# Kernel optimization log

Measured on AMD Instinct MI355X. Metric: run time of the kernel, lower is better.

The kernel has to match this reference:

```python
import jax, jax.numpy as jnp
import numpy as np
from jax import lax


def _conv(x, w, b, pad):
    # x: [B,C,H,W], w: [O,I,kh,kw]
    y = lax.conv_general_dilated(x, w, (1, 1), [(pad, pad), (pad, pad)],
                                 dimension_numbers=('NCHW', 'OIHW', 'NCHW'))
    return y + b[None, :, None, None]


def _maxpool2(x):
    return lax.reduce_window(x, -jnp.inf, lax.max, (1, 1, 2, 2), (1, 1, 2, 2), 'VALID')


def setup_inputs() -> dict:
    key = jax.random.key(0)
    ks = jax.random.split(key, 6)
    N, T, R, D = 8, 64, 9, 512
    x = jax.random.normal(ks[0], (N, T, R, D), dtype=jnp.float32)
    x = x / jnp.linalg.norm(x, axis=-1, keepdims=True)  # ViSiL features are L2-normalized
    w1 = jax.random.normal(ks[1], (32, 1, 3, 3), dtype=jnp.float32) * 0.05
    w2 = jax.random.normal(ks[2], (64, 32, 3, 3), dtype=jnp.float32) * 0.05
    w3 = jax.random.normal(ks[3], (128, 64, 3, 3), dtype=jnp.float32) * 0.05
    w4 = jax.random.normal(ks[4], (1, 128, 1, 1), dtype=jnp.float32) * 0.05
    return {
        'x': x,
        'w1': w1, 'b1': jnp.zeros((32,), jnp.float32),
        'w2': w2, 'b2': jnp.zeros((64,), jnp.float32),
        'w3': w3, 'b3': jnp.zeros((128,), jnp.float32),
        'w4': w4, 'b4': jnp.zeros((1,), jnp.float32),
    }


def reference(x, w1, b1, w2, b2, w3, b3, w4, b4):
    N, T, R, D = x.shape
    # frame-to-frame similarity: region correlation volume + chamfer (max over p, mean over o)
    sim = jnp.einsum('aiok,bjpk->aiopjb', x, x)        # [a,i,o,p,j,b]
    sim = jnp.mean(jnp.max(sim, axis=3), axis=2)        # [a,i,j,b]
    sim = jnp.transpose(sim, (0, 3, 1, 2)).reshape(N * N, 1, T, T)  # '(a b) () i j'
    # VideoComparator CNN head (ZeroPad2d(1) + valid 3x3 conv == 'same' 3x3 conv)
    h = jax.nn.relu(_conv(sim, w1, b1, 1))
    h = _maxpool2(h)
    h = jax.nn.relu(_conv(h, w2, b2, 1))
    h = _maxpool2(h)
    h = jax.nn.relu(_conv(h, w3, b3, 1))
    h = _conv(h, w4, b4, 0)                              # [N*N, 1, T/4, T/4]
    # SimilarityRegularizationLoss(min_val=-1, max_val=1)
    loss = jnp.sum(jax.nn.relu(-(h + 1.0))) + jnp.sum(jax.nn.relu(h - 1.0))
    # Hardtanh, rescale to [0,1], then video-to-video chamfer
    s = jnp.clip(h, -1.0, 1.0) / 2.0 + 0.5
    s = jnp.mean(jnp.max(s, axis=3), axis=2)             # [N*N, 1]
    return s.reshape(N, N), loss
```

## Files before the change

kernel.cpp:

```cpp
#include <hip/hip_runtime.h>

typedef unsigned short u16;
typedef unsigned int u32;
typedef __bf16 bf16x8 __attribute__((ext_vector_type(8)));
typedef u16 u16x8 __attribute__((ext_vector_type(8)));
typedef float f32x4 __attribute__((ext_vector_type(4)));

__device__ __forceinline__ u16 f2bf(float f) {
  u32 u = __float_as_uint(f);
  u32 r = (u + 0x7FFFu + ((u >> 16) & 1u)) >> 16;
  return (u16)r;
}

__device__ __forceinline__ void gload16(const void* g, void* l) {
  typedef __attribute__((address_space(1))) const void gvoid;
  typedef __attribute__((address_space(3))) void lvoid;
  __builtin_amdgcn_global_load_lds((gvoid*)g, (lvoid*)l, 16, 0, 0);
}

__global__ void k_cast(const float* __restrict__ x, char* __restrict__ A8,
                       const float* __restrict__ w2, const float* __restrict__ w3,
                       u16* __restrict__ p2, u16* __restrict__ p3,
                       float* __restrict__ out) {
  int t = blockIdx.x * 256 + threadIdx.x;
  const float4* xp = (const float4*)x + (size_t)t * 2;
  float4 v0 = xp[0], v1 = xp[1];
  int p0 = __builtin_amdgcn_cvt_pk_fp8_f32(v0.x, v0.y, 0, 0);
  p0 = __builtin_amdgcn_cvt_pk_fp8_f32(v0.z, v0.w, p0, 1);
  int p1 = __builtin_amdgcn_cvt_pk_fp8_f32(v1.x, v1.y, 0, 0);
  p1 = __builtin_amdgcn_cvt_pk_fp8_f32(v1.z, v1.w, p1, 1);
  ((int2*)A8)[t] = make_int2(p0, p1);
  if (blockIdx.x == 0 && threadIdx.x < 65) out[threadIdx.x] = 0.f;
  if (t < 18432) {
    int tt = t >> 11, oc = (t >> 5) & 63, ic = t & 31;
    p2[t] = f2bf(w2[(oc * 32 + ic) * 9 + tt]);
  }
  if (t < 73728) {
    int tt = t >> 13, oc = (t >> 6) & 127, ic = t & 63;
    p3[t] = f2bf(w3[(oc * 64 + ic) * 9 + tt]);
  }
}

__global__ __launch_bounds__(256) void k_gemm_smax(const char* __restrict__ A8,
                                                   float* __restrict__ Smax,
                                                   float* __restrict__ Sx) {
  __shared__ char smem[33792];
  float* slab = (float*)smem;
  const int chunk = blockIdx.x & 7, ci = blockIdx.x >> 3;
  const int csz = (chunk < 2) ? 84 : 83;
  if (ci >= csz) return;
  const int tlin = ((chunk < 2) ? 84 * chunk : 168 + 83 * (chunk - 2)) + ci;
  int rb = (int)((73.0f - sqrtf((float)(5329 - 8 * tlin))) * 0.5f);
  while (rb * 36 - rb * (rb - 1) / 2 > tlin) --rb;
  while ((rb + 1) * 36 - (rb + 1) * rb / 2 <= tlin) ++rb;
  const int cb = rb + (tlin - (rb * 36 - rb * (rb - 1) / 2));
  const int rowBase = rb * 128, colBase = cb * 128;
  const int tid = threadIdx.x, wave = tid >> 6, lane = tid & 63;
  const int lr = lane >> 2, lc = lane & 3;
  const int xs = (lr >> 1) & 3;
  const int lrow = lane & 15, lk = lane >> 4;
  const int xr = (lrow >> 1) & 3;
  const int wr = (wave & 1) * 64, wc = (wave >> 1) * 64;

  f32x4 acc[4][4];
#pragma unroll
  for (int rt = 0; rt < 4; ++rt)
#pragma unroll
    for (int ct = 0; ct < 4; ++ct) { f32x4 z = {0.f, 0.f, 0.f, 0.f}; acc[rt][ct] = z; }

  {
    char* As = smem;
    char* Bs = smem + 8192;
#pragma unroll
    for (int ii = 0; ii < 2; ++ii) {
      int r0 = wave * 32 + ii * 16;
      gload16(A8 + (size_t)(rowBase + r0 + lr) * 512 + ((lc ^ xs) * 16), As + r0 * 64);
      gload16(A8 + (size_t)(colBase + r0 + lr) * 512 + ((lc ^ xs) * 16), Bs + r0 * 64);
    }
  }
  __syncthreads();
  for (int k = 0; k < 8; ++k) {
    if (k < 7) {
      char* base = smem + (((k + 1) & 1) << 14);
      char* As = base;
      char* Bs = base + 8192;
      int k0 = (k + 1) * 64;
#pragma unroll
      for (int ii = 0; ii < 2; ++ii) {
        int r0 = wave * 32 + ii * 16;
        gload16(A8 + (size_t)(rowBase + r0 + lr) * 512 + k0 + ((lc ^ xs) * 16),
                As + r0 * 64);
        gload16(A8 + (size_t)(colBase + r0 + lr) * 512 + k0 + ((lc ^ xs) * 16),
                Bs + r0 * 64);
      }
    }
    {
      char* base = smem + ((k & 1) << 14);
      const char* As = base;
      const char* Bs = base + 8192;
#pragma unroll
      for (int s = 0; s < 2; ++s) {
        long af[4], bf[4];
#pragma unroll
        for (int rt = 0; rt < 4; ++rt) {
          int cc = s * 4 + lk;
          int sw = (((cc >> 1) ^ xr) * 16) + ((cc & 1) * 8);
          af[rt] = *(const long*)(As + (wr + rt * 16 + lrow) * 64 + sw);
        }
#pragma unroll
        for (int ct = 0; ct < 4; ++ct) {
          int cc = s * 4 + lk;
          int sw = (((cc >> 1) ^ xr) * 16) + ((cc & 1) * 8);
          bf[ct] = *(const long*)(Bs + (wc + ct * 16 + lrow) * 64 + sw);
        }
#pragma unroll
        for (int rt = 0; rt < 4; ++rt)
#pragma unroll
          for (int ct = 0; ct < 4; ++ct)
            acc[rt][ct] = __builtin_amdgcn_mfma_f32_16x16x32_fp8_fp8(
                af[rt], bf[ct], acc[rt][ct], 0, 0, 0);
      }
    }
    __syncthreads();
  }

  const int g0c = colBase / 9, offc = colBase % 9;
  const int g0r = rowBase / 9, offr = rowBase % 9;
  const int nph = (rb == cb) ? 2 : 4;
  for (int ph = 0; ph < nph; ++ph) {
    __syncthreads();
    if (ph < 2) {
      if ((wave & 1) == ph) {
#pragma unroll
        for (int rt = 0; rt < 4; ++rt)
#pragma unroll
          for (int ct = 0; ct < 4; ++ct)
#pragma unroll
            for (int r = 0; r < 4; ++r)
              slab[(rt * 16 + lk * 4 + r) * 129 + wc + ct * 16 + lrow] = acc[rt][ct][r];
      }
    } else {
      if ((wave >> 1) == ph - 2) {
#pragma unroll
        for (int rt = 0; rt < 4; ++rt)
#pragma unroll
          for (int ct = 0; ct < 4; ++ct)
#pragma unroll
            for (int r = 0; r < 4; ++r)
              slab[(ct * 16 + lrow) * 129 + wr + rt * 16 + lk * 4 + r] = acc[rt][ct][r];
      }
    }
    __syncthreads();
    for (int it = tid; it < 1024; it += 256) {
      int line = it >> 4, s = it & 15;
      float m = -3.0e38f;
      if (ph < 2) {
        int g = g0c + s;
        int cs = 9 * g - colBase, ce = cs + 9;
        cs = cs < 0 ? 0 : cs;
        ce = ce > 128 ? 128 : ce;
        if (cs >= ce) continue;
        const float* p = slab + line * 129;
        for (int c = cs; c < ce; ++c) m = fmaxf(m, p[c]);
        int r = rowBase + ph * 64 + line;
        if (s == 0 && offc != 0) Sx[(size_t)r * 36 + (cb - 1)] = m;
        else Smax[(size_t)r * 512 + g] = m;
      } else {
        int g = g0r + s;
        int rs = 9 * g - rowBase, re = rs + 9;
        rs = rs < 0 ? 0 : rs;
        re = re > 128 ? 128 : re;
        if (rs >= re) continue;
        const float* p = slab + line * 129;
        for (int r2 = rs; r2 < re; ++r2) m = fmaxf(m, p[r2]);
        int cgl = colBase + (ph - 2) * 64 + line;
        if (s == 0 && offr != 0) Sx[(size_t)cgl * 36 + (rb - 1)] = m;
        else Smax[(size_t)cgl * 512 + g] = m;
      }
    }
  }
}

__global__ void k_reduce_o(const float* __restrict__ Smax, const float* __restrict__ Sx,
                           float* __restrict__ sim) {
  int idx = blockIdx.x * 256 + threadIdx.x;
  int j = idx & 63, i = (idx >> 6) & 63, b = (idx >> 12) & 7, a = idx >> 15;
  int g = b * 64 + j;
  int t9 = 9 * g;
  int k = (t9 + 8) >> 7;
  bool part = ((u32)(128 * k - t9 - 1) < 8u);
  const float* p = Smax + (size_t)(a * 576 + i * 9) * 512 + g;
  const float* q = Sx + (size_t)(a * 576 + i * 9) * 36 + (k - 1);
  float s = 0.f;
#pragma unroll
  for (int o = 0; o < 9; ++o) {
    float v = p[o * 512];
    if (part) v = fmaxf(v, q[o * 36]);
    s += v;
  }
  sim[idx] = s * (1.f / 9.f);
}

__global__ __launch_bounds__(256) void k_conv1pool(const float* __restrict__ sim,
                                                   const float* __restrict__ w1,
                                                   const float* __restrict__ b1,
                                                   u16* __restrict__ h1) {
  __shared__ float tin[4096];
  const int pair = blockIdx.x, ocg = blockIdx.y, tid = threadIdx.x;
  const float4* src = (const float4*)(sim + (size_t)pair * 4096);
  for (int i = tid; i < 1024; i += 256) ((float4*)tin)[i] = src[i];
  __syncthreads();
  float wv[8][9], bs[8];
#pragma unroll
  for (int o = 0; o < 8; ++o) {
#pragma unroll
    for (int q = 0; q < 9; ++q) wv[o][q] = w1[(ocg * 8 + o) * 9 + q];
    bs[o] = b1[ocg * 8 + o];
  }
  for (int pp = tid; pp < 1024; pp += 256) {
    int py = pp >> 5, px = pp & 31;
    float m[8];
#pragma unroll
    for (int o = 0; o < 8; ++o) m[o] = 0.f;
#pragma unroll
    for (int dy = 0; dy < 2; ++dy)
#pragma unroll
      for (int dx = 0; dx < 2; ++dx) {
        float s[8];
#pragma unroll
        for (int o = 0; o < 8; ++o) s[o] = bs[o];
        int yy = py * 2 + dy, xx0 = px * 2 + dx;
#pragma unroll
        for (int ky = 0; ky < 3; ++ky) {
          int y = yy + ky - 1;
          if ((unsigned)y < 64u) {
#pragma unroll
            for (int kx = 0; kx < 3; ++kx) {
              int x = xx0 + kx - 1;
              if ((unsigned)x < 64u) {
                float v = tin[y * 64 + x];
#pragma unroll
                for (int o = 0; o < 8; ++o) s[o] += wv[o][ky * 3 + kx] * v;
              }
            }
          }
        }
#pragma unroll
        for (int o = 0; o < 8; ++o) m[o] = fmaxf(m[o], fmaxf(s[o], 0.f));
      }
    u16x8 r;
#pragma unroll
    for (int o = 0; o < 8; ++o) r[o] = f2bf(m[o]);
    *(u16x8*)&h1[(((size_t)pair * 32 + py) * 32 + px) * 32 + ocg * 8] = r;
  }
}

__global__ __launch_bounds__(256) void k_conv2pool(const u16* __restrict__ h1,
                                                   const u16* __restrict__ wp2,
                                                   const float* __restrict__ b2,
                                                   u16* __restrict__ h2) {
  __shared__ u16 tile[18 * 34 * 40];
  const int pair = blockIdx.x, yh = blockIdx.y, tid = threadIdx.x;
  const int wave = tid >> 6, lane = tid & 63, l15 = lane & 15, quad = lane >> 4;
  u16x8 z8 = {0, 0, 0, 0, 0, 0, 0, 0};
  for (int i = tid; i < 3060; i += 256) ((u16x8*)tile)[i] = z8;
  __syncthreads();
  for (int f = tid; f < 1152; f += 256) {
    int i = f >> 6, rem = f & 63, px = rem >> 1, half = rem & 1;
    int gr = yh * 16 - 1 + i;
    if ((unsigned)gr < 32u)
      *(u16x8*)&tile[(i * 34 + 1 + px) * 40 + half * 16] =
          *(const u16x8*)&h1[(((size_t)pair * 32 + gr) * 32 + px) * 32 + half * 16];
  }
  __syncthreads();

  f32x4 acc[8][4];
#pragma unroll
  for (int m = 0; m < 8; ++m)
#pragma unroll
    for (int n = 0; n < 4; ++n) { f32x4 z = {0.f, 0.f, 0.f, 0.f}; acc[m][n] = z; }

  for (int t = 0; t < 9; ++t) {
    int ky = t / 3, kx = t % 3;
    bf16x8 wf[4];
#pragma unroll
    for (int nt = 0; nt < 4; ++nt)
      wf[nt] = *(const bf16x8*)&wp2[((t * 64 + nt * 16 + l15) << 5) + quad * 8];
#pragma unroll
    for (int rr = 0; rr < 4; ++rr)
#pragma unroll
      for (int xh = 0; xh < 2; ++xh) {
        int lr = wave * 4 + rr;
        bf16x8 af = *(const bf16x8*)&tile[((lr + ky) * 34 + xh * 16 + l15 + kx) * 40 +
                                          quad * 8];
#pragma unroll
        for (int nt = 0; nt < 4; ++nt)
          acc[rr * 2 + xh][nt] =
              __builtin_amdgcn_mfma_f32_16x16x32_bf16(af, wf[nt], acc[rr * 2 + xh][nt],
                                                      0, 0, 0);
      }
  }

  float bv[4];
#pragma unroll
  for (int nt = 0; nt < 4; ++nt) bv[nt] = b2[nt * 16 + l15];
#pragma unroll
  for (int rp = 0; rp < 2; ++rp)
#pragma unroll
    for (int xh = 0; xh < 2; ++xh) {
      int py = yh * 8 + wave * 2 + rp;
      int px0 = xh * 8 + quad * 2;
#pragma unroll
      for (int nt = 0; nt < 4; ++nt) {
        f32x4 va = acc[(rp * 2) * 2 + xh][nt], vb = acc[(rp * 2 + 1) * 2 + xh][nt];
        float p0 = fmaxf(fmaxf(fmaxf(va[0], va[1]), fmaxf(vb[0], vb[1])) + bv[nt], 0.f);
        float p1 = fmaxf(fmaxf(fmaxf(va[2], va[3]), fmaxf(vb[2], vb[3])) + bv[nt], 0.f);
        size_t base = (((size_t)pair * 16 + py) * 16 + px0) * 64 + nt * 16 + l15;
        h2[base] = f2bf(p0);
        h2[base + 64] = f2bf(p1);
      }
    }
}

__global__ __launch_bounds__(256) void k_conv34(const u16* __restrict__ h2,
                                                const u16* __restrict__ wp3,
                                                const float* __restrict__ b3,
                                                const float* __restrict__ w4,
                                                const float* __restrict__ b4,
                                                float* __restrict__ out) {
  __shared__ u16 tile[18 * 18 * 72];
  __shared__ float lrow[16];
  __shared__ float lsw[4];
  const int pair = blockIdx.x, tid = threadIdx.x;
  const int wave = tid >> 6, lane = tid & 63, l15 = lane & 15, quad = lane >> 4;
  u16x8 z8 = {0, 0, 0, 0, 0, 0, 0, 0};
  for (int i = tid; i < 2916; i += 256) ((u16x8*)tile)[i] = z8;
  __syncthreads();
  for (int f = tid; f < 2048; f += 256) {
    int row = f >> 7, rem = f & 127, px = rem >> 3, seg = rem & 7;
    *(u16x8*)&tile[((row + 1) * 18 + px + 1) * 72 + seg * 8] =
        *(const u16x8*)&h2[(((size_t)pair * 16 + row) * 16 + px) * 64 + seg * 8];
  }
  __syncthreads();

  f32x4 acc[4][8];
#pragma unroll
  for (int m = 0; m < 4; ++m)
#pragma unroll
    for (int n = 0; n < 8; ++n) { f32x4 z = {0.f, 0.f, 0.f, 0.f}; acc[m][n] = z; }

  for (int t = 0; t < 9; ++t) {
    int ky = t / 3, kx = t % 3;
#pragma unroll
    for (int s = 0; s < 2; ++s) {
      bf16x8 wf[8];
#pragma unroll
      for (int nt = 0; nt < 8; ++nt)
        wf[nt] = *(const bf16x8*)&wp3[((t * 128 + nt * 16 + l15) << 6) + s * 32 +
                                      quad * 8];
#pragma unroll
      for (int yt = 0; yt < 4; ++yt) {
        int y = wave * 4 + yt;
        bf16x8 af = *(const bf16x8*)&tile[((y + ky) * 18 + l15 + kx) * 72 + s * 32 +
                                          quad * 8];
#pragma unroll
        for (int nt = 0; nt < 8; ++nt)
          acc[yt][nt] = __builtin_amdgcn_mfma_f32_16x16x32_bf16(af, wf[nt],
                                                                acc[yt][nt], 0, 0, 0);
      }
    }
  }

  float w4r[8], bvv[8];
#pragma unroll
  for (int nt = 0; nt < 8; ++nt) {
    w4r[nt] = w4[nt * 16 + l15];
    bvv[nt] = b3[nt * 16 + l15];
  }
  float b4v = b4[0];
  float lossacc = 0.f;
#pragma unroll
  for (int yt = 0; yt < 4; ++yt) {
    float hp[4] = {0.f, 0.f, 0.f, 0.f};
#pragma unroll
    for (int nt = 0; nt < 8; ++nt)
#pragma unroll
      for (int r = 0; r < 4; ++r)
        hp[r] += w4r[nt] * fmaxf(acc[yt][nt][r] + bvv[nt], 0.f);
#pragma unroll
    for (int off = 1; off <= 8; off <<= 1)
#pragma unroll
      for (int r = 0; r < 4; ++r) hp[r] += __shfl_xor(hp[r], off, 16);
    float rmax = 0.f, lw = 0.f;
#pragma unroll
    for (int r = 0; r < 4; ++r) {
      float h = hp[r] + b4v;
      lw += fmaxf(-(h + 1.f), 0.f) + fmaxf(h - 1.f, 0.f);
      float sc = fminf(fmaxf(h, -1.f), 1.f) * 0.5f + 0.5f;
      rmax = fmaxf(rmax, sc);
    }
    rmax = fmaxf(rmax, __shfl_xor(rmax, 16));
    rmax = fmaxf(rmax, __shfl_xor(rmax, 32));
    if (lane == 0) lrow[wave * 4 + yt] = rmax;
    lossacc += lw;
  }
#pragma unroll
  for (int off = 32; off >= 1; off >>= 1) lossacc += __shfl_xor(lossacc, off);
  if (lane == 0) lsw[wave] = lossacc * (1.f / 16.f);
  __syncthreads();
  if (tid == 0) {
    float mean = 0.f;
#pragma unroll
    for (int i = 0; i < 16; ++i) mean += lrow[i];
    out[pair] = mean * (1.f / 16.f);
    atomicAdd(out + 64, lsw[0] + lsw[1] + lsw[2] + lsw[3]);
  }
}

extern "C" void kernel_launch(void* const* d_in, const int* in_sizes, int n_in,
                              void* d_out, int out_size, void* d_ws, size_t ws_size,
                              hipStream_t stream) {
  (void)in_sizes; (void)n_in; (void)out_size; (void)ws_size;
  const float* x  = (const float*)d_in[0];
  const float* w1 = (const float*)d_in[1];
  const float* b1 = (const float*)d_in[2];
  const float* w2 = (const float*)d_in[3];
  const float* b2 = (const float*)d_in[4];
  const float* w3 = (const float*)d_in[5];
  const float* b3 = (const float*)d_in[6];
  const float* w4 = (const float*)d_in[7];
  const float* b4 = (const float*)d_in[8];
  float* out = (float*)d_out;

  char* ws = (char*)d_ws;
  char*  A8   = ws;
  float* Smax = (float*)(ws + 2359296);
  float* Sx   = (float*)(ws + 11796480);
  float* sim  = (float*)(ws + 12460032);
  u16*   h1   = (u16*)(ws + 13508608);
  u16*   h2   = (u16*)(ws + 17702912);
  u16*   wp2  = (u16*)(ws + 19800064);
  u16*   wp3  = (u16*)(ws + 19836928);

  k_cast<<<1152, 256, 0, stream>>>(x, A8, w2, w3, wp2, wp3, out);
  k_gemm_smax<<<672, 256, 0, stream>>>(A8, Smax, Sx);
  k_reduce_o<<<1024, 256, 0, stream>>>(Smax, Sx, sim);
  k_conv1pool<<<dim3(64, 4), 256, 0, stream>>>(sim, w1, b1, h1);
  k_conv2pool<<<dim3(64, 2), 256, 0, stream>>>(h1, wp2, b2, h2);
  k_conv34<<<64, 256, 0, stream>>>(h2, wp3, b3, w4, b4, out);
}
```

Measured before the change: 162.6 us.

## Replace double-buffered 64-wide K pipeline with two 256-wide single-buffer stages

The fp8 GEMM main loop previously double-buffered 64-byte K slices in 32 KB of LDS, overlapping the next slice's loads with the current slice's MFMAs. Now LDS grows to 64 KB, and each half of K (256 bytes) is loaded in one batch and then consumed with a wider XOR swizzle. This cuts the number of barriers and loop iterations but removes the load/compute overlap. It also halves the number of blocks that can reside per CU because of the larger shared memory footprint.

```diff
diff --git a/kernel.cpp b/kernel.cpp
--- a/kernel.cpp
+++ b/kernel.cpp
@@ -44,7 +44,7 @@
 __global__ __launch_bounds__(256) void k_gemm_smax(const char* __restrict__ A8,
                                                    float* __restrict__ Smax,
                                                    float* __restrict__ Sx) {
-  __shared__ char smem[33792];
+  __shared__ char smem[65536];
   float* slab = (float*)smem;
   const int chunk = blockIdx.x & 7, ci = blockIdx.x >> 3;
   const int csz = (chunk < 2) ? 84 : 83;
@@ -56,11 +56,12 @@
   const int cb = rb + (tlin - (rb * 36 - rb * (rb - 1) / 2));
   const int rowBase = rb * 128, colBase = cb * 128;
   const int tid = threadIdx.x, wave = tid >> 6, lane = tid & 63;
-  const int lr = lane >> 2, lc = lane & 3;
-  const int xs = (lr >> 1) & 3;
+  const int r2 = lane >> 4, gg = lane & 15;
   const int lrow = lane & 15, lk = lane >> 4;
-  const int xr = (lrow >> 1) & 3;
+  const int xr = lrow & 7;
   const int wr = (wave & 1) * 64, wc = (wave >> 1) * 64;
+  char* As = smem;
+  char* Bs = smem + 32768;
 
   f32x4 acc[4][4];
 #pragma unroll
@@ -68,60 +69,39 @@
 #pragma unroll
     for (int ct = 0; ct < 4; ++ct) { f32x4 z = {0.f, 0.f, 0.f, 0.f}; acc[rt][ct] = z; }
 
-  {
-    char* As = smem;
-    char* Bs = smem + 8192;
-#pragma unroll
-    for (int ii = 0; ii < 2; ++ii) {
-      int r0 = wave * 32 + ii * 16;
-      gload16(A8 + (size_t)(rowBase + r0 + lr) * 512 + ((lc ^ xs) * 16), As + r0 * 64);
-      gload16(A8 + (size_t)(colBase + r0 + lr) * 512 + ((lc ^ xs) * 16), Bs + r0 * 64);
-    }
-  }
-  __syncthreads();
-  for (int k = 0; k < 8; ++k) {
-    if (k < 7) {
-      char* base = smem + (((k + 1) & 1) << 14);
-      char* As = base;
-      char* Bs = base + 8192;
-      int k0 = (k + 1) * 64;
-#pragma unroll
-      for (int ii = 0; ii < 2; ++ii) {
-        int r0 = wave * 32 + ii * 16;
-        gload16(A8 + (size_t)(rowBase + r0 + lr) * 512 + k0 + ((lc ^ xs) * 16),
-                As + r0 * 64);
-        gload16(A8 + (size_t)(colBase + r0 + lr) * 512 + k0 + ((lc ^ xs) * 16),
-                Bs + r0 * 64);
-      }
-    }
-    {
-      char* base = smem + ((k & 1) << 14);
-      const char* As = base;
-      const char* Bs = base + 8192;
-#pragma unroll
-      for (int s = 0; s < 2; ++s) {
-        long af[4], bf[4];
-#pragma unroll
-        for (int rt = 0; rt < 4; ++rt) {
-          int cc = s * 4 + lk;
-          int sw = (((cc >> 1) ^ xr) * 16) + ((cc & 1) * 8);
-          af[rt] = *(const long*)(As + (wr + rt * 16 + lrow) * 64 + sw);
-        }
-#pragma unroll
-        for (int ct = 0; ct < 4; ++ct) {
-          int cc = s * 4 + lk;
-          int sw = (((cc >> 1) ^ xr) * 16) + ((cc & 1) * 8);
-          bf[ct] = *(const long*)(Bs + (wc + ct * 16 + lrow) * 64 + sw);
-        }
-#pragma unroll
-        for (int rt = 0; rt < 4; ++rt)
-#pragma unroll
-          for (int ct = 0; ct < 4; ++ct)
-            acc[rt][ct] = __builtin_amdgcn_mfma_f32_16x16x32_fp8_fp8(
-                af[rt], bf[ct], acc[rt][ct], 0, 0, 0);
-      }
-    }
+  for (int half = 0; half < 2; ++half) {
+    const int k0 = half * 256;
     __syncthreads();
+#pragma unroll
+    for (int ii = 0; ii < 8; ++ii) {
+      int r0 = wave * 32 + ii * 4;
+      int row = r0 + r2;
+      gload16(A8 + (size_t)(rowBase + row) * 512 + k0 + ((gg ^ (row & 7)) * 16),
+              As + r0 * 256);
+      gload16(A8 + (size_t)(colBase + row) * 512 + k0 + ((gg ^ (row & 7)) * 16),
+              Bs + r0 * 256);
+    }
+    __syncthreads();
+#pragma unroll
+    for (int cc = 0; cc < 8; ++cc) {
+      const int gi = cc * 2 + (lk >> 1);
+      const int sub = (lk & 1) * 8;
+      long af[4], bf[4];
+#pragma unroll
+      for (int rt = 0; rt < 4; ++rt)
+        af[rt] = *(const long*)(As + (wr + rt * 16 + lrow) * 256 +
+                                ((gi ^ xr) * 16) + sub);
+#pragma unroll
+      for (int ct = 0; ct < 4; ++ct)
+        bf[ct] = *(const long*)(Bs + (wc + ct * 16 + lrow) * 256 +
+                                ((gi ^ xr) * 16) + sub);
+#pragma unroll
+      for (int rt = 0; rt < 4; ++rt)
+#pragma unroll
+        for (int ct = 0; ct < 4; ++ct)
+          acc[rt][ct] = __builtin_amdgcn_mfma_f32_16x16x32_fp8_fp8(
+              af[rt], bf[ct], acc[rt][ct], 0, 0, 0);
+    }
   }
 
   const int g0c = colBase / 9, offc = colBase % 9;
@@ -172,7 +152,7 @@
         re = re > 128 ? 128 : re;
         if (rs >= re) continue;
         const float* p = slab + line * 129;
-        for (int r2 = rs; r2 < re; ++r2) m = fmaxf(m, p[r2]);
+        for (int r3 = rs; r3 < re; ++r3) m = fmaxf(m, p[r3]);
         int cgl = colBase + (ph - 2) * 64 + line;
         if (s == 0 && offr != 0) Sx[(size_t)cgl * 36 + (rb - 1)] = m;
         else Smax[(size_t)cgl * 512 + g] = m;
```

Result: no change. 161.4 us (-0.7%).
